# Performance work log

Measured on AMD Instinct MI355X. Metric: run time of the kernel, lower is better.

## Reference

```python
import jax, jax.numpy as jnp
import numpy as np

N, D, H, DFF, NH = 8192, 128, 256, 2048, 2
HD = D // NH
DEG = 32
E = N * DEG
LN_EPS = 1e-5


def setup_inputs() -> dict:
    key = jax.random.key(0)
    ks = jax.random.split(key, 20)
    s = 0.02
    return {
        "x": jax.random.normal(ks[0], (N, D), jnp.float32),
        "edge_index": jax.random.randint(ks[1], (2, E), 0, N, jnp.int64),
        "beta": jnp.ones((), jnp.float32),  # AGNNConv learnable beta, init 1
        "in_proj_w": jax.random.normal(ks[2], (3 * D, D), jnp.float32) * s,
        "in_proj_b": jnp.zeros((3 * D,), jnp.float32),
        "out_proj_w": jax.random.normal(ks[3], (D, D), jnp.float32) * s,
        "out_proj_b": jnp.zeros((D,), jnp.float32),
        "ln1_g": jnp.ones((D,), jnp.float32),
        "ln1_b": jnp.zeros((D,), jnp.float32),
        "ff1_w": jax.random.normal(ks[4], (DFF, D), jnp.float32) * s,
        "ff1_b": jnp.zeros((DFF,), jnp.float32),
        "ff2_w": jax.random.normal(ks[5], (D, DFF), jnp.float32) * s,
        "ff2_b": jnp.zeros((D,), jnp.float32),
        "ln2_g": jnp.ones((D,), jnp.float32),
        "ln2_b": jnp.zeros((D,), jnp.float32),
        "fc_w": jax.random.normal(ks[6], (H, D), jnp.float32) * s,
        "fc_b": jnp.zeros((H,), jnp.float32),
        "head_w": jax.random.normal(ks[7], (2, H), jnp.float32) * s,
        "head_b": jnp.zeros((2,), jnp.float32),
    }


def _layernorm(x, g, b):
    mu = jnp.mean(x, axis=-1, keepdims=True)
    var = jnp.mean((x - mu) ** 2, axis=-1, keepdims=True)
    return (x - mu) * jax.lax.rsqrt(var + LN_EPS) * g + b


def _agnn(x, edge_index, beta):
    # PyG AGNNConv: add self-loops, cosine-sim attention, segment softmax over targets
    n = x.shape[0]
    loop = jnp.arange(n, dtype=edge_index.dtype)
    src = jnp.concatenate([edge_index[0], loop])  # message source j
    dst = jnp.concatenate([edge_index[1], loop])  # aggregation target i
    xn = x / jnp.maximum(jnp.linalg.norm(x, axis=-1, keepdims=True), 1e-12)
    alpha = beta * jnp.sum(xn[dst] * xn[src], axis=-1)  # [E+N]
    m = jax.ops.segment_max(alpha, dst, num_segments=n)
    e = jnp.exp(alpha - m[dst])
    z = jax.ops.segment_sum(e, dst, num_segments=n)
    w = e / z[dst]
    return jax.ops.segment_sum(w[:, None] * x[src], dst, num_segments=n)


def reference(x, edge_index, beta, in_proj_w, in_proj_b, out_proj_w, out_proj_b,
              ln1_g, ln1_b, ff1_w, ff1_b, ff2_w, ff2_b, ln2_g, ln2_b,
              fc_w, fc_b, head_w, head_b):
    h = _agnn(x, edge_index, beta)  # [N, D]
    # transformer sees shape [N, 1, D] with batch_first=False -> seq over all N nodes
    qkv = h @ in_proj_w.T + in_proj_b  # [N, 3D]
    q, k, v = jnp.split(qkv, 3, axis=-1)
    q = q.reshape(N, NH, HD).transpose(1, 0, 2)  # [h, N, hd]
    k = k.reshape(N, NH, HD).transpose(1, 0, 2)
    v = v.reshape(N, NH, HD).transpose(1, 0, 2)
    scores = jnp.einsum('hnd,hmd->hnm', q, k) / jnp.sqrt(jnp.float32(HD))
    attn = jax.nn.softmax(scores, axis=-1)
    o = jnp.einsum('hnm,hmd->hnd', attn, v).transpose(1, 0, 2).reshape(N, D)
    o = o @ out_proj_w.T + out_proj_b
    h = _layernorm(h + o, ln1_g, ln1_b)  # post-LN (norm_first=False)
    ff = jax.nn.relu(h @ ff1_w.T + ff1_b) @ ff2_w.T + ff2_b
    h = _layernorm(h + ff, ln2_g, ln2_b)
    h = jax.nn.relu(h @ fc_w.T + fc_b)
    return h @ head_w.T + head_b  # [N, 2]
```

## Files before the change

kernel.cpp:

```cpp
#include <hip/hip_runtime.h>


typedef __attribute__((ext_vector_type(4))) float  f32x4;
typedef __attribute__((ext_vector_type(8))) __bf16 bf16x8;

#define DEV __device__ __forceinline__

DEV __bf16 f2bf(float f) {
  union { float f; unsigned u; } v; v.f = f;
  unsigned r = v.u + 0x7FFFu + ((v.u >> 16) & 1u);
  union { unsigned short s; __bf16 b; } o; o.s = (unsigned short)(r >> 16);
  return o.b;
}

DEV f32x4 mfma16(bf16x8 a, bf16x8 b, f32x4 c) {
  return __builtin_amdgcn_mfma_f32_16x16x32_bf16(a, b, c, 0, 0, 0);
}

DEV bf16x8 ones8() {
  union { unsigned short s[8]; bf16x8 v; } u;
#pragma unroll
  for (int i = 0; i < 8; i++) u.s[i] = 0x3F80;
  return u.v;
}

#define GLD16(gp, lp) __builtin_amdgcn_global_load_lds(                        \
    (const __attribute__((address_space(1))) void*)(gp),                       \
    (__attribute__((address_space(3))) void*)(lp), 16, 0, 0)


__global__ __launch_bounds__(256) void k_norm(const float* __restrict__ x,
                                              float* __restrict__ inv) {
  int lane = threadIdx.x & 63, w = threadIdx.x >> 6;
  int row = blockIdx.x * 4 + w;
  float2 v = ((const float2*)(x + (size_t)row * 128))[lane];
  float s = v.x * v.x + v.y * v.y;
#pragma unroll
  for (int m = 1; m < 64; m <<= 1) s += __shfl_xor(s, m);
  if (lane == 0) inv[row] = 1.f / fmaxf(sqrtf(s), 1e-12f);
}

__global__ __launch_bounds__(256) void k_cvt5(
    const float* __restrict__ s0, const float* __restrict__ s1,
    const float* __restrict__ s2, const float* __restrict__ s3,
    const float* __restrict__ s4, __bf16* d0, __bf16* d1, __bf16* d2,
    __bf16* d3, __bf16* d4, int n0, int n1, int n2, int n3, int n4) {
  int t = blockIdx.x * 256 + threadIdx.x;
  if (t < n0) { d0[t] = f2bf(s0[t]); return; } t -= n0;
  if (t < n1) { d1[t] = f2bf(s1[t]); return; } t -= n1;
  if (t < n2) { d2[t] = f2bf(s2[t]); return; } t -= n2;
  if (t < n3) { d3[t] = f2bf(s3[t]); return; } t -= n3;
  if (t < n4) { d4[t] = f2bf(s4[t]); }
}

__global__ void k_count(const int* __restrict__ ei, int* __restrict__ counts,
                        int E) {
  int e = blockIdx.x * 256 + threadIdx.x;
  if (e < E) atomicAdd(&counts[ei[E + e]], 1);
}

__global__ __launch_bounds__(256) void k_scan(const int* __restrict__ counts,
                                              int* __restrict__ offs,
                                              int* __restrict__ cursor) {
  __shared__ int sums[256];
  int t = threadIdx.x, base = t * 32;
  int s = 0;
  for (int i = 0; i < 32; i++) s += counts[base + i];
  sums[t] = s;
  __syncthreads();
  for (int off = 1; off < 256; off <<= 1) {
    int v = (t >= off) ? sums[t - off] : 0;
    __syncthreads();
    sums[t] += v;
    __syncthreads();
  }
  int run = sums[t] - s;
  for (int i = 0; i < 32; i++) {
    offs[base + i] = run; cursor[base + i] = run;
    run += counts[base + i];
  }
  if (t == 255) offs[8192] = run;
}

__global__ void k_scatter(const int* __restrict__ ei, int* __restrict__ cursor,
                          int* __restrict__ csr, int E) {
  int e = blockIdx.x * 256 + threadIdx.x;
  if (e < E) {
    int dst = ei[E + e];
    int pos = atomicAdd(&cursor[dst], 1);
    csr[pos] = ei[e];
  }
}

__global__ __launch_bounds__(256) void k_agnn(
    const float* __restrict__ x, const int* __restrict__ csr,
    const int* __restrict__ offs, const float* __restrict__ inv,
    const float* __restrict__ betap, float* __restrict__ hf,
    __bf16* __restrict__ hb) {
  int lane = threadIdx.x & 63, w = threadIdx.x >> 6;
  int dst = blockIdx.x * 4 + w;
  float beta = *betap;
  float2 xd = ((const float2*)(x + (size_t)dst * 128))[lane];
  float invd = inv[dst];
  float sd = xd.x * xd.x + xd.y * xd.y;
#pragma unroll
  for (int m = 1; m < 64; m <<= 1) sd += __shfl_xor(sd, m);
  float z = __expf(beta * sd * invd * invd);
  float ax = z * xd.x, ay = z * xd.y;
  int e0 = offs[dst], e1 = offs[dst + 1];
  int e = e0;
  for (; e + 2 <= e1; e += 2) {
    int s0 = csr[e], s1 = csr[e + 1];
    float2 xa = ((const float2*)(x + (size_t)s0 * 128))[lane];
    float2 xb = ((const float2*)(x + (size_t)s1 * 128))[lane];
    float ia = inv[s0], ib = inv[s1];
    float da = xd.x * xa.x + xd.y * xa.y;
    float db = xd.x * xb.x + xd.y * xb.y;
#pragma unroll
    for (int m = 1; m < 64; m <<= 1) {
      da += __shfl_xor(da, m);
      db += __shfl_xor(db, m);
    }
    float sa = __expf(beta * da * invd * ia);
    float sb = __expf(beta * db * invd * ib);
    z += sa + sb;
    ax += sa * xa.x + sb * xb.x;
    ay += sa * xa.y + sb * xb.y;
  }
  if (e < e1) {
    int s0 = csr[e];
    float2 xa = ((const float2*)(x + (size_t)s0 * 128))[lane];
    float da = xd.x * xa.x + xd.y * xa.y;
#pragma unroll
    for (int m = 1; m < 64; m <<= 1) da += __shfl_xor(da, m);
    float sa = __expf(beta * da * invd * inv[s0]);
    z += sa; ax += sa * xa.x; ay += sa * xa.y;
  }
  float r = 1.f / z;
  ax *= r; ay *= r;
  float2 o; o.x = ax; o.y = ay;
  ((float2*)(hf + (size_t)dst * 128))[lane] = o;
  hb[(size_t)dst * 128 + 2 * lane]     = f2bf(ax);
  hb[(size_t)dst * 128 + 2 * lane + 1] = f2bf(ay);
}

__global__ __launch_bounds__(256, 2) void k_gemm(
    const __bf16* __restrict__ A, const __bf16* __restrict__ B,
    const float* __restrict__ bias, float* __restrict__ Cf,
    __bf16* __restrict__ Cb, float* __restrict__ Cpart, int M, int N, int K,
    int relu) {
  __shared__ __bf16 As[128 * 64];
  __shared__ __bf16 Bs[128 * 64];
  const int tid = threadIdx.x, lane = tid & 63, wid = tid >> 6;
  const int wm = wid & 1, wn = wid >> 1;
  const int bm = blockIdx.x * 128, bn = blockIdx.y * 128;
  const int kz = blockIdx.z, nkz = gridDim.z;
  const int kchunk = K / nkz, k0beg = kz * kchunk, k0end = k0beg + kchunk;
  const int lr = lane >> 3, lc8 = (lane & 7) * 8;
  const int l15 = lane & 15, quad = lane >> 4, kq = quad * 8;

  f32x4 acc[4][4] = {};
  const __bf16* Ab = A + (size_t)(bm + lr) * K + lc8;
  const __bf16* Bb = B + (size_t)(bn + lr) * K + lc8;

  for (int k0 = k0beg; k0 < k0end; k0 += 64) {
#pragma unroll
    for (int i = 0; i < 4; i++) {
      int j = wid * 4 + i;
      GLD16(Ab + (size_t)(8 * j) * K + k0, &As[j * 512]);
      GLD16(Bb + (size_t)(8 * j) * K + k0, &Bs[j * 512]);
    }
    __syncthreads();
    const int ar = (wm * 64 + l15) * 64 + kq;
    const int br = (wn * 64 + l15) * 64 + kq;
#pragma unroll
    for (int kk = 0; kk < 2; kk++) {
      bf16x8 a[4], b[4];
#pragma unroll
      for (int mt = 0; mt < 4; mt++)
        a[mt] = *(const bf16x8*)&As[ar + mt * 1024 + kk * 32];
#pragma unroll
      for (int nt = 0; nt < 4; nt++)
        b[nt] = *(const bf16x8*)&Bs[br + nt * 1024 + kk * 32];
#pragma unroll
      for (int mt = 0; mt < 4; mt++)
#pragma unroll
        for (int nt = 0; nt < 4; nt++)
          acc[mt][nt] = mfma16(a[mt], b[nt], acc[mt][nt]);
    }
    __syncthreads();
  }
  const int col0 = bn + wn * 64 + l15;
  const int row0 = bm + wm * 64 + quad * 4;
  if (Cpart) {
    float* P = Cpart + (size_t)kz * M * N;
#pragma unroll
    for (int mt = 0; mt < 4; mt++)
#pragma unroll
      for (int nt = 0; nt < 4; nt++)
#pragma unroll
        for (int r = 0; r < 4; r++)
          P[(size_t)(row0 + mt * 16 + r) * N + col0 + nt * 16] = acc[mt][nt][r];
  } else {
#pragma unroll
    for (int nt = 0; nt < 4; nt++) {
      float bv = bias[col0 + nt * 16];
#pragma unroll
      for (int mt = 0; mt < 4; mt++)
#pragma unroll
        for (int r = 0; r < 4; r++) {
          float v = acc[mt][nt][r] + bv;
          if (relu) v = fmaxf(v, 0.f);
          size_t idx = (size_t)(row0 + mt * 16 + r) * N + col0 + nt * 16;
          if (Cf) Cf[idx] = v;
          if (Cb) Cb[idx] = f2bf(v);
        }
    }
  }
}

__global__ __launch_bounds__(256) void k_qkvprep(const float* __restrict__ qkv,
                                                 __bf16* __restrict__ Qb,
                                                 __bf16* __restrict__ Kb,
                                                 __bf16* __restrict__ Vtb) {
  __shared__ __bf16 tile[64][130];
  int nb = blockIdx.x * 64;
  int t = threadIdx.x;
  const float qscale = 0.125f * 1.44269504089f;
  for (int rr = 0; rr < 64; rr++) {
    int row = nb + rr;
    float v = qkv[(size_t)row * 384 + t];
    if (t < 128) {
      Qb[((size_t)(t >> 6) * 8192 + row) * 64 + (t & 63)] = f2bf(v * qscale);
    } else {
      int c = t - 128;
      Kb[((size_t)(c >> 6) * 8192 + row) * 64 + (c & 63)] = f2bf(v);
    }
  }
  int col = t & 127, rh = t >> 7;
  for (int rr = 0; rr < 64; rr += 2) {
    int row = rr + rh;
    tile[row][col] = f2bf(qkv[(size_t)(nb + row) * 384 + 256 + col]);
  }
  __syncthreads();
  int hd = t >> 1, half = t & 1;
  __bf16 tmp[32];
#pragma unroll
  for (int i = 0; i < 32; i++) tmp[i] = tile[half * 32 + i][hd];
  __bf16* dst = Vtb + (size_t)hd * 8192 + nb + half * 32;
#pragma unroll
  for (int i = 0; i < 4; i++)
    *(bf16x8*)(dst + i * 8) = *(const bf16x8*)(tmp + i * 8);
}

__global__ __launch_bounds__(256, 4) void k_attn(
    const __bf16* __restrict__ Qb, const __bf16* __restrict__ Kb,
    const __bf16* __restrict__ Vtb, __bf16* __restrict__ Opart,
    float* __restrict__ Lpart) {
  __shared__ __bf16 Ks[4096];
  __shared__ __bf16 Vs[4096];
  __shared__ __bf16 Ps[4][32 * 88];

  const int tid = threadIdx.x, lane = tid & 63, w = tid >> 6;
  const int qt = blockIdx.x, h = blockIdx.y, kz = blockIdx.z;
  const int qbase = qt * 128;
  const int l15 = lane & 15, quad = lane >> 4;
  const int lofs = lane * 8;

  const __bf16* Qg = Qb + ((size_t)h * 8192 + qbase) * 64;
  const __bf16* Kg = Kb + (size_t)h * 8192 * 64;
  const __bf16* Vg = Vtb + (size_t)h * 64 * 8192;
  const bf16x8 vone = ones8();

#pragma unroll
  for (int i = 0; i < 2; i++) {
    int j = w * 2 + i;
    __bf16* dstb = (j < 4) ? &Ks[j * 1024] : &Vs[(j - 4) * 1024];
#pragma unroll
    for (int hh = 0; hh < 2; hh++)
      GLD16(Qg + (size_t)(j * 16 + l15) * 64 + hh * 32 + quad * 8,
            dstb + hh * 512);
  }
  __syncthreads();
  bf16x8 aq[2][2];
#pragma unroll
  for (int s = 0; s < 2; s++) {
    int j = w * 2 + s;
    const __bf16* base = (j < 4) ? &Ks[j * 1024] : &Vs[(j - 4) * 1024];
    aq[s][0] = *(const bf16x8*)&base[lofs];
    aq[s][1] = *(const bf16x8*)&base[512 + lofs];
  }
  __syncthreads();

  f32x4 o[2][4] = {};
  f32x4 lacc[2] = {};
  const int kstart = kz * 1024;

  for (int kt = 0; kt < 16; kt++) {
    int kb = kstart + kt * 64;
#pragma unroll
    for (int hh = 0; hh < 2; hh++) {
      GLD16(Kg + (size_t)(kb + w * 16 + l15) * 64 + hh * 32 + quad * 8,
            &Ks[w * 1024 + hh * 512]);
      GLD16(Vg + (size_t)(w * 16 + l15) * 8192 + kb + hh * 32 + quad * 8,
            &Vs[w * 1024 + hh * 512]);
    }
    __syncthreads();

#pragma unroll
    for (int mt = 0; mt < 4; mt++) {
      bf16x8 k0 = *(const bf16x8*)&Ks[mt * 1024 + lofs];
      bf16x8 k1 = *(const bf16x8*)&Ks[mt * 1024 + 512 + lofs];
#pragma unroll
      for (int s = 0; s < 2; s++) {
        f32x4 St = {};
        St = mfma16(k0, aq[s][0], St);
        St = mfma16(k1, aq[s][1], St);
        union { float f; unsigned u; } p0, p1, p2, p3;
        p0.f = __builtin_amdgcn_exp2f(St[0]);
        p1.f = __builtin_amdgcn_exp2f(St[1]);
        p2.f = __builtin_amdgcn_exp2f(St[2]);
        p3.f = __builtin_amdgcn_exp2f(St[3]);
        uint2 pk;
        pk.x = (p0.u >> 16) | (p1.u & 0xFFFF0000u);
        pk.y = (p2.u >> 16) | (p3.u & 0xFFFF0000u);
        *(uint2*)&Ps[w][(s * 16 + l15) * 88 + mt * 16 + quad * 4] = pk;
      }
    }
    bf16x8 vf[4][2];
#pragma unroll
    for (int nd = 0; nd < 4; nd++) {
      vf[nd][0] = *(const bf16x8*)&Vs[nd * 1024 + lofs];
      vf[nd][1] = *(const bf16x8*)&Vs[nd * 1024 + 512 + lofs];
    }
#pragma unroll
    for (int s = 0; s < 2; s++) {
      bf16x8 ap0 = *(const bf16x8*)&Ps[w][(s * 16 + l15) * 88 + quad * 8];
      bf16x8 ap1 = *(const bf16x8*)&Ps[w][(s * 16 + l15) * 88 + 32 + quad * 8];
      lacc[s] = mfma16(ap0, vone, lacc[s]);
      lacc[s] = mfma16(ap1, vone, lacc[s]);
#pragma unroll
      for (int nd = 0; nd < 4; nd++) {
        o[s][nd] = mfma16(ap0, vf[nd][0], o[s][nd]);
        o[s][nd] = mfma16(ap1, vf[nd][1], o[s][nd]);
      }
    }
    __syncthreads();
  }

  const size_t bpart = (size_t)(h * 8 + kz);
#pragma unroll
  for (int s = 0; s < 2; s++) {
#pragma unroll
    for (int nd = 0; nd < 4; nd++)
#pragma unroll
      for (int r = 0; r < 4; r++) {
        int row = qbase + w * 32 + s * 16 + quad * 4 + r;
        Opart[(bpart * 8192 + row) * 64 + nd * 16 + l15] = f2bf(o[s][nd][r]);
      }
    if (l15 == 0) {
#pragma unroll
      for (int r = 0; r < 4; r++) {
        int row = qbase + w * 32 + s * 16 + quad * 4 + r;
        Lpart[bpart * 8192 + row] = lacc[s][r];
      }
    }
  }
}

__global__ __launch_bounds__(256) void k_attn_combine(
    const __bf16* __restrict__ Opart, const float* __restrict__ Lpart,
    __bf16* __restrict__ obf) {
  int t = blockIdx.x * 256 + threadIdx.x;
  int d = t & 63;
  int n = (t >> 6) & 8191;
  int h = t >> 19;
  float acc = 0.f, L = 0.f;
#pragma unroll
  for (int z = 0; z < 8; z++) {
    size_t idx = (size_t)(h * 8 + z) * 8192 + n;
    acc += (float)Opart[idx * 64 + d];
    L += Lpart[idx];
  }
  obf[(size_t)n * 128 + h * 64 + d] = f2bf(acc / L);
}

__global__ __launch_bounds__(256) void k_addln(
    const float* __restrict__ A, const float* __restrict__ Bv,
    const float* __restrict__ g, const float* __restrict__ bt,
    float* __restrict__ outf, __bf16* __restrict__ outb) {
  int lane = threadIdx.x & 63, w = threadIdx.x >> 6;
  int row = blockIdx.x * 4 + w;
  float2 a = ((const float2*)(A + (size_t)row * 128))[lane];
  float2 b = ((const float2*)(Bv + (size_t)row * 128))[lane];
  float vx = a.x + b.x, vy = a.y + b.y;
  float s = vx + vy;
#pragma unroll
  for (int m = 1; m < 64; m <<= 1) s += __shfl_xor(s, m);
  float mu = s * (1.f / 128.f);
  float dx = vx - mu, dy = vy - mu;
  float q = dx * dx + dy * dy;
#pragma unroll
  for (int m = 1; m < 64; m <<= 1) q += __shfl_xor(q, m);
  float rstd = rsqrtf(q * (1.f / 128.f) + 1e-5f);
  float2 gg = ((const float2*)g)[lane];
  float2 bb = ((const float2*)bt)[lane];
  float y0 = dx * rstd * gg.x + bb.x;
  float y1 = dy * rstd * gg.y + bb.y;
  if (outf) {
    float2 o; o.x = y0; o.y = y1;
    ((float2*)(outf + (size_t)row * 128))[lane] = o;
  }
  if (outb) {
    outb[(size_t)row * 128 + 2 * lane]     = f2bf(y0);
    outb[(size_t)row * 128 + 2 * lane + 1] = f2bf(y1);
  }
}

__global__ __launch_bounds__(256) void k_addln4(
    const float* __restrict__ A, const float* __restrict__ part,
    const float* __restrict__ pbias, const float* __restrict__ g,
    const float* __restrict__ bt, __bf16* __restrict__ outb) {
  int lane = threadIdx.x & 63, w = threadIdx.x >> 6;
  int row = blockIdx.x * 4 + w;
  float2 a = ((const float2*)(A + (size_t)row * 128))[lane];
  float2 pb = ((const float2*)pbias)[lane];
  float sx = 0.f, sy = 0.f;
#pragma unroll
  for (int z = 0; z < 4; z++) {
    float2 p =
        ((const float2*)(part + (size_t)z * 1048576 + (size_t)row * 128))[lane];
    sx += p.x; sy += p.y;
  }
  float vx = a.x + pb.x + sx, vy = a.y + pb.y + sy;
  float s = vx + vy;
#pragma unroll
  for (int m = 1; m < 64; m <<= 1) s += __shfl_xor(s, m);
  float mu = s * (1.f / 128.f);
  float dx = vx - mu, dy = vy - mu;
  float q = dx * dx + dy * dy;
#pragma unroll
  for (int m = 1; m < 64; m <<= 1) q += __shfl_xor(q, m);
  float rstd = rsqrtf(q * (1.f / 128.f) + 1e-5f);
  float2 gg = ((const float2*)g)[lane];
  float2 bb = ((const float2*)bt)[lane];
  outb[(size_t)row * 128 + 2 * lane]     = f2bf(dx * rstd * gg.x + bb.x);
  outb[(size_t)row * 128 + 2 * lane + 1] = f2bf(dy * rstd * gg.y + bb.y);
}

__global__ __launch_bounds__(256) void k_head(const float* __restrict__ fc,
                                              const float* __restrict__ hw,
                                              const float* __restrict__ hb,
                                              float* __restrict__ out) {
  int lane = threadIdx.x & 63, w = threadIdx.x >> 6;
  int row = blockIdx.x * 4 + w;
  float4 v  = ((const float4*)(fc + (size_t)row * 256))[lane];
  float4 w0 = ((const float4*)hw)[lane];
  float4 w1 = ((const float4*)(hw + 256))[lane];
  float p0 = v.x * w0.x + v.y * w0.y + v.z * w0.z + v.w * w0.w;
  float p1 = v.x * w1.x + v.y * w1.y + v.z * w1.z + v.w * w1.w;
#pragma unroll
  for (int m = 1; m < 64; m <<= 1) {
    p0 += __shfl_xor(p0, m);
    p1 += __shfl_xor(p1, m);
  }
  if (lane == 0) {
    out[(size_t)row * 2]     = p0 + hb[0];
    out[(size_t)row * 2 + 1] = p1 + hb[1];
  }
}

extern "C" void kernel_launch(void* const* d_in, const int* in_sizes, int n_in,
                              void* d_out, int out_size, void* d_ws,
                              size_t ws_size, hipStream_t stream) {
  const float* x     = (const float*)d_in[0];
  const int*   ei    = (const int*)d_in[1];
  const float* beta  = (const float*)d_in[2];
  const float* in_w  = (const float*)d_in[3];
  const float* in_b  = (const float*)d_in[4];
  const float* out_w = (const float*)d_in[5];
  const float* out_b = (const float*)d_in[6];
  const float* ln1g  = (const float*)d_in[7];
  const float* ln1b  = (const float*)d_in[8];
  const float* ff1w  = (const float*)d_in[9];
  const float* ff1b  = (const float*)d_in[10];
  const float* ff2w  = (const float*)d_in[11];
  const float* ff2b  = (const float*)d_in[12];
  const float* ln2g  = (const float*)d_in[13];
  const float* ln2b  = (const float*)d_in[14];
  const float* fcw   = (const float*)d_in[15];
  const float* fcb   = (const float*)d_in[16];
  const float* hw    = (const float*)d_in[17];
  const float* hbias = (const float*)d_in[18];
  float* out = (float*)d_out;
  const int N = 8192;
  const int E = in_sizes[1] / 2;

  char* wsp = (char*)d_ws;
  size_t off = 0;
  auto alloc = [&](size_t b) -> void* {
    void* p = wsp + off;
    off = (off + b + 255) & ~(size_t)255;
    return p;
  };

  float*  inv     = (float*)alloc((size_t)N * 4);
  int*    counts  = (int*)alloc((size_t)N * 4);
  int*    offs    = (int*)alloc((size_t)(N + 1) * 4);
  int*    cursor  = (int*)alloc((size_t)N * 4);
  int*    csr     = (int*)alloc((size_t)E * 4);
  float*  h_f     = (float*)alloc((size_t)N * 128 * 4);
  __bf16* h_b     = (__bf16*)alloc((size_t)N * 128 * 2);
  __bf16* o_b     = (__bf16*)alloc((size_t)N * 128 * 2);
  float*  oproj   = (float*)alloc((size_t)N * 128 * 4);
  float*  h1_f    = (float*)alloc((size_t)N * 128 * 4);
  __bf16* h1_b    = (__bf16*)alloc((size_t)N * 128 * 2);
  __bf16* h2_b    = (__bf16*)alloc((size_t)N * 128 * 2);
  float*  fco     = (float*)alloc((size_t)N * 256 * 4);
  float*  Lpart   = (float*)alloc((size_t)16 * N * 4);
  __bf16* w_in    = (__bf16*)alloc((size_t)384 * 128 * 2);
  __bf16* w_out   = (__bf16*)alloc((size_t)128 * 128 * 2);
  __bf16* w_ff1   = (__bf16*)alloc((size_t)2048 * 128 * 2);
  __bf16* w_ff2   = (__bf16*)alloc((size_t)128 * 2048 * 2);
  __bf16* w_fc    = (__bf16*)alloc((size_t)256 * 128 * 2);
  char*   bigA    = (char*)alloc((size_t)16 * N * 64 * 4);
  __bf16* Opart   = (__bf16*)bigA;
  __bf16* ff1o    = (__bf16*)bigA;
  char*   bigB    = (char*)alloc((size_t)18874368);
  float*  qkv     = (float*)bigB;
  __bf16* Qb      = (__bf16*)(bigB + 12582912);
  __bf16* Kb      = (__bf16*)(bigB + 12582912 + 2097152);
  __bf16* Vtb     = (__bf16*)(bigB + 12582912 + 2 * 2097152);
  float*  ff2part = (float*)bigB;
  (void)ws_size; (void)n_in; (void)out_size;

  hipMemsetAsync(counts, 0, (size_t)N * 4, stream);
  k_norm<<<N / 4, 256, 0, stream>>>(x, inv);
  {
    int n0 = 384 * 128, n1 = 128 * 128, n2 = 2048 * 128, n3 = 128 * 2048,
        n4 = 256 * 128;
    int tot = n0 + n1 + n2 + n3 + n4;
    k_cvt5<<<(tot + 255) / 256, 256, 0, stream>>>(
        in_w, out_w, ff1w, ff2w, fcw, w_in, w_out, w_ff1, w_ff2, w_fc, n0, n1,
        n2, n3, n4);
  }
  k_count<<<(E + 255) / 256, 256, 0, stream>>>(ei, counts, E);
  k_scan<<<1, 256, 0, stream>>>(counts, offs, cursor);
  k_scatter<<<(E + 255) / 256, 256, 0, stream>>>(ei, cursor, csr, E);
  k_agnn<<<N / 4, 256, 0, stream>>>(x, csr, offs, inv, beta, h_f, h_b);

  k_gemm<<<dim3(64, 3, 1), 256, 0, stream>>>(h_b, w_in, in_b, qkv, nullptr,
                                             nullptr, N, 384, 128, 0);
  k_qkvprep<<<128, 256, 0, stream>>>(qkv, Qb, Kb, Vtb);
  k_attn<<<dim3(64, 2, 8), 256, 0, stream>>>(Qb, Kb, Vtb, Opart, Lpart);
  k_attn_combine<<<(2 * N * 64) / 256, 256, 0, stream>>>(Opart, Lpart, o_b);
  k_gemm<<<dim3(64, 1, 1), 256, 0, stream>>>(o_b, w_out, out_b, oproj, nullptr,
                                             nullptr, N, 128, 128, 0);
  k_addln<<<N / 4, 256, 0, stream>>>(h_f, oproj, ln1g, ln1b, h1_f, h1_b);
  k_gemm<<<dim3(64, 16, 1), 256, 0, stream>>>(h1_b, w_ff1, ff1b, nullptr, ff1o,
                                              nullptr, N, 2048, 128, 1);
  k_gemm<<<dim3(64, 1, 4), 256, 0, stream>>>(ff1o, w_ff2, nullptr, nullptr,
                                             nullptr, ff2part, N, 128, 2048, 0);
  k_addln4<<<N / 4, 256, 0, stream>>>(h1_f, ff2part, ff2b, ln2g, ln2b, h2_b);
  k_gemm<<<dim3(64, 2, 1), 256, 0, stream>>>(h2_b, w_fc, fcb, fco, nullptr,
                                             nullptr, N, 256, 128, 1);
  k_head<<<N / 4, 256, 0, stream>>>(fco, hw, hbias, out);
}
```

Measured before the change: 287.2 us.

## Fuse prep kernels, QKV epilogue, out-proj+LN1, and fc+head into fewer launches

Merges norm, count-zeroing and weight conversion into one prep kernel, which replaces a memset and two launches. The QKV GEMM now writes bf16 Q/K/V (including the V transpose) directly, so the fp32 qkv buffer and the separate prep kernel are gone. The attention partial combine is fused with the output projection, residual add and first LayerNorm, and the fc GEMM is fused with the ReLU and the 2-wide head. Together these cut launches and intermediate global traffic. The fused kernels run only 128 blocks, which may underfill the GPU, and LN1 now uses a single-pass variance.

```diff
diff --git a/kernel.cpp b/kernel.cpp
--- a/kernel.cpp
+++ b/kernel.cpp
@@ -6,10 +6,14 @@
 
 #define DEV __device__ __forceinline__
 
-DEV __bf16 f2bf(float f) {
+DEV unsigned short f2bf_bits(float f) {
   union { float f; unsigned u; } v; v.f = f;
   unsigned r = v.u + 0x7FFFu + ((v.u >> 16) & 1u);
-  union { unsigned short s; __bf16 b; } o; o.s = (unsigned short)(r >> 16);
+  return (unsigned short)(r >> 16);
+}
+
+DEV __bf16 f2bf(float f) {
+  union { unsigned short s; __bf16 b; } o; o.s = f2bf_bits(f);
   return o.b;
 }
 
@@ -22,6 +26,15 @@
 #pragma unroll
   for (int i = 0; i < 8; i++) u.s[i] = 0x3F80;
   return u.v;
+}
+
+DEV void ub8(bf16x8 v, float* f) {
+  union { bf16x8 v; unsigned short s[8]; } u; u.v = v;
+#pragma unroll
+  for (int i = 0; i < 8; i++) {
+    union { unsigned u; float f; } w; w.u = (unsigned)u.s[i] << 16;
+    f[i] = w.f;
+  }
 }
 
 #define GLD16(gp, lp) __builtin_amdgcn_global_load_lds(                        \
@@ -29,29 +42,35 @@
     (__attribute__((address_space(3))) void*)(lp), 16, 0, 0)
 
 
-__global__ __launch_bounds__(256) void k_norm(const float* __restrict__ x,
-                                              float* __restrict__ inv) {
-  int lane = threadIdx.x & 63, w = threadIdx.x >> 6;
-  int row = blockIdx.x * 4 + w;
-  float2 v = ((const float2*)(x + (size_t)row * 128))[lane];
-  float s = v.x * v.x + v.y * v.y;
-#pragma unroll
-  for (int m = 1; m < 64; m <<= 1) s += __shfl_xor(s, m);
-  if (lane == 0) inv[row] = 1.f / fmaxf(sqrtf(s), 1e-12f);
-}
-
-__global__ __launch_bounds__(256) void k_cvt5(
-    const float* __restrict__ s0, const float* __restrict__ s1,
-    const float* __restrict__ s2, const float* __restrict__ s3,
-    const float* __restrict__ s4, __bf16* d0, __bf16* d1, __bf16* d2,
-    __bf16* d3, __bf16* d4, int n0, int n1, int n2, int n3, int n4) {
-  int t = blockIdx.x * 256 + threadIdx.x;
+__global__ __launch_bounds__(256) void k_prep(
+    const float* __restrict__ x, float* __restrict__ inv,
+    int* __restrict__ counts, const float* __restrict__ s0,
+    const float* __restrict__ s1, const float* __restrict__ s2,
+    const float* __restrict__ s3, const float* __restrict__ s4, __bf16* d0,
+    __bf16* d1, __bf16* d2, __bf16* d3, __bf16* d4) {
+  const int n0 = 384 * 128, n1 = 128 * 128, n2 = 2048 * 128, n3 = 128 * 2048,
+            n4 = 256 * 128;
+  if (blockIdx.x < 2048) {
+    int lane = threadIdx.x & 63, w = threadIdx.x >> 6;
+    int row = blockIdx.x * 4 + w;
+    float2 v = ((const float2*)(x + (size_t)row * 128))[lane];
+    float s = v.x * v.x + v.y * v.y;
+#pragma unroll
+    for (int m = 1; m < 64; m <<= 1) s += __shfl_xor(s, m);
+    if (lane == 0) {
+      inv[row] = 1.f / fmaxf(sqrtf(s), 1e-12f);
+      counts[row] = 0;
+    }
+    return;
+  }
+  int t = (blockIdx.x - 2048) * 256 + threadIdx.x;
   if (t < n0) { d0[t] = f2bf(s0[t]); return; } t -= n0;
   if (t < n1) { d1[t] = f2bf(s1[t]); return; } t -= n1;
   if (t < n2) { d2[t] = f2bf(s2[t]); return; } t -= n2;
   if (t < n3) { d3[t] = f2bf(s3[t]); return; } t -= n3;
   if (t < n4) { d4[t] = f2bf(s4[t]); }
 }
+
 
 __global__ void k_count(const int* __restrict__ ei, int* __restrict__ counts,
                         int E) {
@@ -219,38 +238,96 @@
   }
 }
 
-__global__ __launch_bounds__(256) void k_qkvprep(const float* __restrict__ qkv,
-                                                 __bf16* __restrict__ Qb,
-                                                 __bf16* __restrict__ Kb,
-                                                 __bf16* __restrict__ Vtb) {
-  __shared__ __bf16 tile[64][130];
-  int nb = blockIdx.x * 64;
-  int t = threadIdx.x;
+__global__ __launch_bounds__(256, 2) void k_gemm_qkv(
+    const __bf16* __restrict__ A, const __bf16* __restrict__ B,
+    const float* __restrict__ bias, __bf16* __restrict__ Qb,
+    __bf16* __restrict__ Kb, __bf16* __restrict__ Vtb) {
+  __shared__ __bf16 smem[17408];
+  __bf16* As = smem;
+  __bf16* Bs = smem + 8192;
+  const int K = 128;
+  const int tid = threadIdx.x, lane = tid & 63, wid = tid >> 6;
+  const int wm = wid & 1, wn = wid >> 1;
+  const int bm = blockIdx.x * 128, y = blockIdx.y, bn = y * 128;
+  const int lr = lane >> 3, lc8 = (lane & 7) * 8;
+  const int l15 = lane & 15, quad = lane >> 4, kq = quad * 8;
   const float qscale = 0.125f * 1.44269504089f;
-  for (int rr = 0; rr < 64; rr++) {
-    int row = nb + rr;
-    float v = qkv[(size_t)row * 384 + t];
-    if (t < 128) {
-      Qb[((size_t)(t >> 6) * 8192 + row) * 64 + (t & 63)] = f2bf(v * qscale);
-    } else {
-      int c = t - 128;
-      Kb[((size_t)(c >> 6) * 8192 + row) * 64 + (c & 63)] = f2bf(v);
-    }
-  }
-  int col = t & 127, rh = t >> 7;
-  for (int rr = 0; rr < 64; rr += 2) {
-    int row = rr + rh;
-    tile[row][col] = f2bf(qkv[(size_t)(nb + row) * 384 + 256 + col]);
-  }
-  __syncthreads();
-  int hd = t >> 1, half = t & 1;
-  __bf16 tmp[32];
-#pragma unroll
-  for (int i = 0; i < 32; i++) tmp[i] = tile[half * 32 + i][hd];
-  __bf16* dst = Vtb + (size_t)hd * 8192 + nb + half * 32;
-#pragma unroll
-  for (int i = 0; i < 4; i++)
-    *(bf16x8*)(dst + i * 8) = *(const bf16x8*)(tmp + i * 8);
+
+  f32x4 acc[4][4] = {};
+  const __bf16* Ab = A + (size_t)(bm + lr) * K + lc8;
+  const __bf16* Bb = B + (size_t)(bn + lr) * K + lc8;
+
+  for (int k0 = 0; k0 < 128; k0 += 64) {
+#pragma unroll
+    for (int i = 0; i < 4; i++) {
+      int j = wid * 4 + i;
+      GLD16(Ab + (size_t)(8 * j) * K + k0, &As[j * 512]);
+      GLD16(Bb + (size_t)(8 * j) * K + k0, &Bs[j * 512]);
+    }
+    __syncthreads();
+    const int ar = (wm * 64 + l15) * 64 + kq;
+    const int br = (wn * 64 + l15) * 64 + kq;
+#pragma unroll
+    for (int kk = 0; kk < 2; kk++) {
+      bf16x8 a[4], b[4];
+#pragma unroll
+      for (int mt = 0; mt < 4; mt++)
+        a[mt] = *(const bf16x8*)&As[ar + mt * 1024 + kk * 32];
+#pragma unroll
+      for (int nt = 0; nt < 4; nt++)
+        b[nt] = *(const bf16x8*)&Bs[br + nt * 1024 + kk * 32];
+#pragma unroll
+      for (int mt = 0; mt < 4; mt++)
+#pragma unroll
+        for (int nt = 0; nt < 4; nt++)
+          acc[mt][nt] = mfma16(a[mt], b[nt], acc[mt][nt]);
+    }
+    __syncthreads();
+  }
+
+  if (y < 2) {
+    __bf16* D = (y == 0) ? Qb : Kb;
+    float sc = (y == 0) ? qscale : 1.f;
+    int h = wn;
+#pragma unroll
+    for (int nt = 0; nt < 4; nt++) {
+      int c = wn * 64 + nt * 16 + l15;
+      float bv = bias[bn + c];
+      int d = nt * 16 + l15;
+#pragma unroll
+      for (int mt = 0; mt < 4; mt++)
+#pragma unroll
+        for (int r = 0; r < 4; r++) {
+          int row = bm + wm * 64 + mt * 16 + quad * 4 + r;
+          D[(size_t)h * 524288 + (size_t)row * 64 + d] =
+              f2bf((acc[mt][nt][r] + bv) * sc);
+        }
+    }
+  } else {
+#pragma unroll
+    for (int nt = 0; nt < 4; nt++) {
+      int c = wn * 64 + nt * 16 + l15;
+      float bv = bias[bn + c];
+#pragma unroll
+      for (int mt = 0; mt < 4; mt++)
+#pragma unroll
+        for (int r = 0; r < 4; r++) {
+          int nl = wm * 64 + mt * 16 + quad * 4 + r;
+          smem[nl * 136 + c] = f2bf(acc[mt][nt][r] + bv);
+        }
+    }
+    __syncthreads();
+    int d = tid >> 1, nh = tid & 1;
+    __bf16* dst = Vtb + (size_t)d * 8192 + bm + nh * 64;
+#pragma unroll
+    for (int i = 0; i < 8; i++) {
+      union { unsigned short s[8]; bf16x8 v; } u;
+#pragma unroll
+      for (int e = 0; e < 8; e++)
+        u.s[e] = *(const unsigned short*)&smem[(nh * 64 + i * 8 + e) * 136 + d];
+      *(bf16x8*)(dst + i * 8) = u.v;
+    }
+  }
 }
 
 __global__ __launch_bounds__(256, 4) void k_attn(
@@ -368,53 +445,124 @@
   }
 }
 
-__global__ __launch_bounds__(256) void k_attn_combine(
+__global__ __launch_bounds__(256) void k_oproj_ln(
     const __bf16* __restrict__ Opart, const float* __restrict__ Lpart,
-    __bf16* __restrict__ obf) {
-  int t = blockIdx.x * 256 + threadIdx.x;
-  int d = t & 63;
-  int n = (t >> 6) & 8191;
-  int h = t >> 19;
-  float acc = 0.f, L = 0.f;
-#pragma unroll
-  for (int z = 0; z < 8; z++) {
-    size_t idx = (size_t)(h * 8 + z) * 8192 + n;
-    acc += (float)Opart[idx * 64 + d];
-    L += Lpart[idx];
-  }
-  obf[(size_t)n * 128 + h * 64 + d] = f2bf(acc / L);
-}
-
-__global__ __launch_bounds__(256) void k_addln(
-    const float* __restrict__ A, const float* __restrict__ Bv,
-    const float* __restrict__ g, const float* __restrict__ bt,
-    float* __restrict__ outf, __bf16* __restrict__ outb) {
-  int lane = threadIdx.x & 63, w = threadIdx.x >> 6;
-  int row = blockIdx.x * 4 + w;
-  float2 a = ((const float2*)(A + (size_t)row * 128))[lane];
-  float2 b = ((const float2*)(Bv + (size_t)row * 128))[lane];
-  float vx = a.x + b.x, vy = a.y + b.y;
-  float s = vx + vy;
-#pragma unroll
-  for (int m = 1; m < 64; m <<= 1) s += __shfl_xor(s, m);
-  float mu = s * (1.f / 128.f);
-  float dx = vx - mu, dy = vy - mu;
-  float q = dx * dx + dy * dy;
-#pragma unroll
-  for (int m = 1; m < 64; m <<= 1) q += __shfl_xor(q, m);
-  float rstd = rsqrtf(q * (1.f / 128.f) + 1e-5f);
-  float2 gg = ((const float2*)g)[lane];
-  float2 bb = ((const float2*)bt)[lane];
-  float y0 = dx * rstd * gg.x + bb.x;
-  float y1 = dy * rstd * gg.y + bb.y;
-  if (outf) {
-    float2 o; o.x = y0; o.y = y1;
-    ((float2*)(outf + (size_t)row * 128))[lane] = o;
-  }
-  if (outb) {
-    outb[(size_t)row * 128 + 2 * lane]     = f2bf(y0);
-    outb[(size_t)row * 128 + 2 * lane + 1] = f2bf(y1);
-  }
+    const __bf16* __restrict__ Wo, const float* __restrict__ ob,
+    const float* __restrict__ hf, const float* __restrict__ g,
+    const float* __restrict__ bt, float* __restrict__ h1f,
+    __bf16* __restrict__ h1b) {
+  __shared__ __bf16 Af[4 * 2048];
+  __shared__ __bf16 Bf[8 * 2048];
+  __shared__ float scr1[64][2], scr2[64][2];
+  const int tid = threadIdx.x, lane = tid & 63, w = tid >> 6;
+  const int l15 = lane & 15, quad = lane >> 4;
+  const int lofs = lane * 8;
+  const int bm = blockIdx.x * 64;
+  const int wm = w & 1, wn = w >> 1;
+
+#pragma unroll
+  for (int f = 0; f < 2; f++) {
+    int j = w * 2 + f;
+#pragma unroll
+    for (int kq = 0; kq < 4; kq++)
+      GLD16(Wo + (size_t)(j * 16 + l15) * 128 + kq * 32 + quad * 8,
+            &Bf[j * 2048 + kq * 512]);
+  }
+  {
+    int n = bm + w * 16 + l15;
+    float L0 = 0.f, L1 = 0.f;
+#pragma unroll
+    for (int z = 0; z < 8; z++) {
+      L0 += Lpart[(size_t)z * 8192 + n];
+      L1 += Lpart[(size_t)(8 + z) * 8192 + n];
+    }
+    float r0 = 1.f / L0, r1 = 1.f / L1;
+#pragma unroll
+    for (int kq = 0; kq < 4; kq++) {
+      int hh = kq >> 1;
+      int d0 = (kq & 1) * 32 + quad * 8;
+      float acc8[8] = {};
+#pragma unroll
+      for (int z = 0; z < 8; z++) {
+        bf16x8 t = *(const bf16x8*)&Opart[((size_t)(hh * 8 + z) * 8192 + n) *
+                                              64 + d0];
+        float f[8];
+        ub8(t, f);
+#pragma unroll
+        for (int e = 0; e < 8; e++) acc8[e] += f[e];
+      }
+      float rh = hh ? r1 : r0;
+      union { unsigned short s[8]; bf16x8 v; } u;
+#pragma unroll
+      for (int e = 0; e < 8; e++) u.s[e] = f2bf_bits(acc8[e] * rh);
+      *(bf16x8*)&Af[w * 2048 + kq * 512 + lane * 8] = u.v;
+    }
+  }
+  __syncthreads();
+
+  f32x4 acc[2][4] = {};
+#pragma unroll
+  for (int kq = 0; kq < 4; kq++) {
+    bf16x8 a[2], b[4];
+#pragma unroll
+    for (int mt = 0; mt < 2; mt++)
+      a[mt] = *(const bf16x8*)&Af[(wm * 2 + mt) * 2048 + kq * 512 + lofs];
+#pragma unroll
+    for (int nt = 0; nt < 4; nt++)
+      b[nt] = *(const bf16x8*)&Bf[(wn * 4 + nt) * 2048 + kq * 512 + lofs];
+#pragma unroll
+    for (int mt = 0; mt < 2; mt++)
+#pragma unroll
+      for (int nt = 0; nt < 4; nt++)
+        acc[mt][nt] = mfma16(a[mt], b[nt], acc[mt][nt]);
+  }
+
+  float v[2][4][4];
+#pragma unroll
+  for (int mt = 0; mt < 2; mt++)
+#pragma unroll
+    for (int r = 0; r < 4; r++) {
+      int row = bm + wm * 32 + mt * 16 + quad * 4 + r;
+      float s1 = 0.f, s2 = 0.f;
+#pragma unroll
+      for (int nt = 0; nt < 4; nt++) {
+        int col = wn * 64 + nt * 16 + l15;
+        float val = acc[mt][nt][r] + ob[col] + hf[(size_t)row * 128 + col];
+        v[mt][nt][r] = val;
+        s1 += val;
+        s2 += val * val;
+      }
+#pragma unroll
+      for (int msk = 1; msk < 16; msk <<= 1) {
+        s1 += __shfl_xor(s1, msk);
+        s2 += __shfl_xor(s2, msk);
+      }
+      if (l15 == 0) {
+        int rl = wm * 32 + mt * 16 + quad * 4 + r;
+        scr1[rl][wn] = s1;
+        scr2[rl][wn] = s2;
+      }
+    }
+  __syncthreads();
+#pragma unroll
+  for (int mt = 0; mt < 2; mt++)
+#pragma unroll
+    for (int r = 0; r < 4; r++) {
+      int rl = wm * 32 + mt * 16 + quad * 4 + r;
+      int row = bm + rl;
+      float S1 = scr1[rl][0] + scr1[rl][1];
+      float S2 = scr2[rl][0] + scr2[rl][1];
+      float mu = S1 * (1.f / 128.f);
+      float var = S2 * (1.f / 128.f) - mu * mu;
+      float rstd = rsqrtf(var + 1e-5f);
+#pragma unroll
+      for (int nt = 0; nt < 4; nt++) {
+        int col = wn * 64 + nt * 16 + l15;
+        float y = (v[mt][nt][r] - mu) * rstd * g[col] + bt[col];
+        h1f[(size_t)row * 128 + col] = y;
+        h1b[(size_t)row * 128 + col] = f2bf(y);
+      }
+    }
 }
 
 __global__ __launch_bounds__(256) void k_addln4(
@@ -448,25 +596,77 @@
   outb[(size_t)row * 128 + 2 * lane + 1] = f2bf(dy * rstd * gg.y + bb.y);
 }
 
-__global__ __launch_bounds__(256) void k_head(const float* __restrict__ fc,
-                                              const float* __restrict__ hw,
-                                              const float* __restrict__ hb,
-                                              float* __restrict__ out) {
-  int lane = threadIdx.x & 63, w = threadIdx.x >> 6;
-  int row = blockIdx.x * 4 + w;
-  float4 v  = ((const float4*)(fc + (size_t)row * 256))[lane];
-  float4 w0 = ((const float4*)hw)[lane];
-  float4 w1 = ((const float4*)(hw + 256))[lane];
-  float p0 = v.x * w0.x + v.y * w0.y + v.z * w0.z + v.w * w0.w;
-  float p1 = v.x * w1.x + v.y * w1.y + v.z * w1.z + v.w * w1.w;
-#pragma unroll
-  for (int m = 1; m < 64; m <<= 1) {
-    p0 += __shfl_xor(p0, m);
-    p1 += __shfl_xor(p1, m);
-  }
-  if (lane == 0) {
-    out[(size_t)row * 2]     = p0 + hb[0];
-    out[(size_t)row * 2 + 1] = p1 + hb[1];
+__global__ __launch_bounds__(256) void k_fc_head(
+    const __bf16* __restrict__ A, const __bf16* __restrict__ Wfc,
+    const float* __restrict__ fcb, const float* __restrict__ hw,
+    const float* __restrict__ hb, float* __restrict__ out) {
+  __shared__ __bf16 Af[4 * 2048];
+  __shared__ __bf16 Bf[16 * 2048];
+  __shared__ float scr0[64][2], scr1[64][2];
+  const int tid = threadIdx.x, lane = tid & 63, w = tid >> 6;
+  const int l15 = lane & 15, quad = lane >> 4;
+  const int lofs = lane * 8;
+  const int bm = blockIdx.x * 64;
+  const int wm = w & 1, wn = w >> 1;
+
+#pragma unroll
+  for (int kq = 0; kq < 4; kq++)
+    GLD16(A + (size_t)(bm + w * 16 + l15) * 128 + kq * 32 + quad * 8,
+          &Af[w * 2048 + kq * 512]);
+#pragma unroll
+  for (int f = 0; f < 4; f++) {
+    int j = w * 4 + f;
+#pragma unroll
+    for (int kq = 0; kq < 4; kq++)
+      GLD16(Wfc + (size_t)(j * 16 + l15) * 128 + kq * 32 + quad * 8,
+            &Bf[j * 2048 + kq * 512]);
+  }
+  __syncthreads();
+
+  f32x4 acc[2][8] = {};
+#pragma unroll
+  for (int kq = 0; kq < 4; kq++) {
+    bf16x8 a[2], b[8];
+#pragma unroll
+    for (int mt = 0; mt < 2; mt++)
+      a[mt] = *(const bf16x8*)&Af[(wm * 2 + mt) * 2048 + kq * 512 + lofs];
+#pragma unroll
+    for (int nt = 0; nt < 8; nt++)
+      b[nt] = *(const bf16x8*)&Bf[(wn * 8 + nt) * 2048 + kq * 512 + lofs];
+#pragma unroll
+    for (int mt = 0; mt < 2; mt++)
+#pragma unroll
+      for (int nt = 0; nt < 8; nt++)
+        acc[mt][nt] = mfma16(a[mt], b[nt], acc[mt][nt]);
+  }
+
+#pragma unroll
+  for (int mt = 0; mt < 2; mt++)
+#pragma unroll
+    for (int r = 0; r < 4; r++) {
+      float p0 = 0.f, p1 = 0.f;
+#pragma unroll
+      for (int nt = 0; nt < 8; nt++) {
+        int col = wn * 128 + nt * 16 + l15;
+        float vv = fmaxf(acc[mt][nt][r] + fcb[col], 0.f);
+        p0 += vv * hw[col];
+        p1 += vv * hw[256 + col];
+      }
+#pragma unroll
+      for (int msk = 1; msk < 16; msk <<= 1) {
+        p0 += __shfl_xor(p0, msk);
+        p1 += __shfl_xor(p1, msk);
+      }
+      if (l15 == 0) {
+        int rl = wm * 32 + mt * 16 + quad * 4 + r;
+        scr0[rl][wn] = p0;
+        scr1[rl][wn] = p1;
+      }
+    }
+  __syncthreads();
+  if (tid < 64) {
+    out[(size_t)(bm + tid) * 2]     = scr0[tid][0] + scr0[tid][1] + hb[0];
+    out[(size_t)(bm + tid) * 2 + 1] = scr1[tid][0] + scr1[tid][1] + hb[1];
   }
 }
 
@@ -511,12 +711,9 @@
   int*    csr     = (int*)alloc((size_t)E * 4);
   float*  h_f     = (float*)alloc((size_t)N * 128 * 4);
   __bf16* h_b     = (__bf16*)alloc((size_t)N * 128 * 2);
-  __bf16* o_b     = (__bf16*)alloc((size_t)N * 128 * 2);
-  float*  oproj   = (float*)alloc((size_t)N * 128 * 4);
   float*  h1_f    = (float*)alloc((size_t)N * 128 * 4);
   __bf16* h1_b    = (__bf16*)alloc((size_t)N * 128 * 2);
   __bf16* h2_b    = (__bf16*)alloc((size_t)N * 128 * 2);
-  float*  fco     = (float*)alloc((size_t)N * 256 * 4);
   float*  Lpart   = (float*)alloc((size_t)16 * N * 4);
   __bf16* w_in    = (__bf16*)alloc((size_t)384 * 128 * 2);
   __bf16* w_out   = (__bf16*)alloc((size_t)128 * 128 * 2);
@@ -526,43 +723,28 @@
   char*   bigA    = (char*)alloc((size_t)16 * N * 64 * 4);
   __bf16* Opart   = (__bf16*)bigA;
   __bf16* ff1o    = (__bf16*)bigA;
-  char*   bigB    = (char*)alloc((size_t)18874368);
-  float*  qkv     = (float*)bigB;
-  __bf16* Qb      = (__bf16*)(bigB + 12582912);
-  __bf16* Kb      = (__bf16*)(bigB + 12582912 + 2097152);
-  __bf16* Vtb     = (__bf16*)(bigB + 12582912 + 2 * 2097152);
+  char*   bigB    = (char*)alloc((size_t)16777216);
+  __bf16* Qb      = (__bf16*)bigB;
+  __bf16* Kb      = (__bf16*)(bigB + 2097152);
+  __bf16* Vtb     = (__bf16*)(bigB + 2 * 2097152);
   float*  ff2part = (float*)bigB;
   (void)ws_size; (void)n_in; (void)out_size;
 
-  hipMemsetAsync(counts, 0, (size_t)N * 4, stream);
-  k_norm<<<N / 4, 256, 0, stream>>>(x, inv);
-  {
-    int n0 = 384 * 128, n1 = 128 * 128, n2 = 2048 * 128, n3 = 128 * 2048,
-        n4 = 256 * 128;
-    int tot = n0 + n1 + n2 + n3 + n4;
-    k_cvt5<<<(tot + 255) / 256, 256, 0, stream>>>(
-        in_w, out_w, ff1w, ff2w, fcw, w_in, w_out, w_ff1, w_ff2, w_fc, n0, n1,
-        n2, n3, n4);
-  }
+  k_prep<<<4784, 256, 0, stream>>>(x, inv, counts, in_w, out_w, ff1w, ff2w,
+                                   fcw, w_in, w_out, w_ff1, w_ff2, w_fc);
   k_count<<<(E + 255) / 256, 256, 0, stream>>>(ei, counts, E);
   k_scan<<<1, 256, 0, stream>>>(counts, offs, cursor);
   k_scatter<<<(E + 255) / 256, 256, 0, stream>>>(ei, cursor, csr, E);
   k_agnn<<<N / 4, 256, 0, stream>>>(x, csr, offs, inv, beta, h_f, h_b);
 
-  k_gemm<<<dim3(64, 3, 1), 256, 0, stream>>>(h_b, w_in, in_b, qkv, nullptr,
-                                             nullptr, N, 384, 128, 0);
-  k_qkvprep<<<128, 256, 0, stream>>>(qkv, Qb, Kb, Vtb);
+  k_gemm_qkv<<<dim3(64, 3), 256, 0, stream>>>(h_b, w_in, in_b, Qb, Kb, Vtb);
   k_attn<<<dim3(64, 2, 8), 256, 0, stream>>>(Qb, Kb, Vtb, Opart, Lpart);
-  k_attn_combine<<<(2 * N * 64) / 256, 256, 0, stream>>>(Opart, Lpart, o_b);
-  k_gemm<<<dim3(64, 1, 1), 256, 0, stream>>>(o_b, w_out, out_b, oproj, nullptr,
-                                             nullptr, N, 128, 128, 0);
-  k_addln<<<N / 4, 256, 0, stream>>>(h_f, oproj, ln1g, ln1b, h1_f, h1_b);
+  k_oproj_ln<<<128, 256, 0, stream>>>(Opart, Lpart, w_out, out_b, h_f, ln1g,
+                                      ln1b, h1_f, h1_b);
   k_gemm<<<dim3(64, 16, 1), 256, 0, stream>>>(h1_b, w_ff1, ff1b, nullptr, ff1o,
                                               nullptr, N, 2048, 128, 1);
   k_gemm<<<dim3(64, 1, 4), 256, 0, stream>>>(ff1o, w_ff2, nullptr, nullptr,
                                              nullptr, ff2part, N, 128, 2048, 0);
   k_addln4<<<N / 4, 256, 0, stream>>>(h1_f, ff2part, ff2b, ln2g, ln2b, h2_b);
-  k_gemm<<<dim3(64, 2, 1), 256, 0, stream>>>(h2_b, w_fc, fcb, fco, nullptr,
-                                             nullptr, N, 256, 128, 1);
-  k_head<<<N / 4, 256, 0, stream>>>(fco, hw, hbias, out);
-}
+  k_fc_head<<<128, 256, 0, stream>>>(h2_b, w_fc, fcb, hw, hbias, out);
+}
```

New measurement: 265.1 us. 1.08x faster.
